# Performance work log

Measured on AMD Instinct MI355X. Metric: run time of the kernel, lower is better.

## Reference

```python
import jax, jax.numpy as jnp
import numpy as np

B, S, E, H = 8, 1024, 1024, 16
DK = E // H  # = n_wires = 64


def setup_inputs() -> dict:
    key = jax.random.key(0)
    k1, k2, k3 = jax.random.split(key, 3)
    x = jax.random.normal(k1, (B, S, E), dtype=jnp.float32)
    # trainable per-wire RX angles (shared across tokens and heads, as in QLayer)
    theta = jax.random.normal(k2, (DK,), dtype=jnp.float32)
    # combine_heads: nn.Linear(E, E, bias=False) -> weight [E, E], y = x @ W.T
    W_combine = (jax.random.normal(k3, (E, E), dtype=jnp.float32) / np.float32(np.sqrt(E)))
    return {"x": x, "theta": theta, "W_combine": W_combine}


def reference(x, theta, W_combine):
    # Quantum projection: per wire, RX(x_i) then RX(theta_i) on |0>, measure PauliZ.
    # RX(a)RX(b) = RX(a+b); <Z> of RX(a)|0> = cos(a)  =>  proj = cos(x + theta).
    b, s, e = x.shape
    xh = x.reshape(b, s, H, DK)            # [B, S, H, DK]
    proj = jnp.cos(xh + theta)             # product-state circuit, fully vectorized
    qkv = proj.transpose(0, 2, 1, 3)       # [B, H, S, DK]; q = k = v = proj

    scale = jnp.float32(1.0 / np.sqrt(DK))
    scores = jnp.einsum('bhqd,bhkd->bhqk', qkv, qkv) * scale  # [B, H, S, S]
    attn = jax.nn.softmax(scores, axis=-1)  # dropout disabled (eval / p=0)
    out = jnp.einsum('bhqk,bhkd->bhqd', attn, qkv)            # [B, H, S, DK]
    out = out.transpose(0, 2, 1, 3).reshape(b, s, e)          # [B, S, E]
    return out @ W_combine.T
```

## Files before the change

### kernel.cpp

```cpp
#include <hip/hip_runtime.h>
#include <hip/hip_bf16.h>
#include <stdint.h>

typedef float  f32x4   __attribute__((ext_vector_type(4)));
typedef float  f32x16  __attribute__((ext_vector_type(16)));
typedef __bf16 bf16x8  __attribute__((ext_vector_type(8)));
typedef __bf16 bf16x4  __attribute__((ext_vector_type(4)));

static constexpr int NB = 8, NS = 1024, NE = 1024, NH = 16;

#define MFMA16(a, b, c) __builtin_amdgcn_mfma_f32_16x16x32_bf16((a), (b), (c), 0, 0, 0)
#define MFMA32(a, b, c) __builtin_amdgcn_mfma_f32_32x32x16_bf16((a), (b), (c), 0, 0, 0)

__device__ __forceinline__ void gload_lds16(const void* g, void* l) {
    __builtin_amdgcn_global_load_lds(
        (const __attribute__((address_space(1))) void*)g,
        (__attribute__((address_space(3))) void*)l, 16, 0, 0);
}

__device__ __forceinline__ uint32_t cvt_pk_bf16(float lo, float hi) {
    uint32_t r;
    asm("v_cvt_pk_bf16_f32 %0, %1, %2" : "=v"(r) : "v"(lo), "v"(hi));
    return r;
}
__device__ __forceinline__ void pl32swap(uint32_t& a, uint32_t& b) {
    asm volatile("v_permlane32_swap_b32 %0, %1" : "+v"(a), "+v"(b));
}
__device__ __forceinline__ float exp2_raw(float x) {
    float r;
    asm("v_exp_f32 %0, %1" : "=v"(r) : "v"(x));
    return r;
}

__global__ __launch_bounds__(256) void k_proj(const float* __restrict__ x,
                                              const float* __restrict__ theta,
                                              __bf16* __restrict__ proj,
                                              __bf16* __restrict__ projT) {
    __shared__ float sm[64][65];
    const int bid  = blockIdx.x;
    const int bh   = bid >> 4;
    const int st0  = (bid & 15) << 6;
    const int b    = bh >> 4, h = bh & 15;
    const int t    = threadIdx.x;
    const int srow = t >> 2;
    const int j4   = t & 3;

    const float* xrow = x + ((size_t)(b * NS + st0 + srow)) * NE + h * 64;
    __bf16* prow = proj + ((size_t)bh * NS + st0 + srow) * 64;

#pragma unroll
    for (int k = 0; k < 4; ++k) {
        const int d = k * 16 + j4 * 4;
        float4 xv = *(const float4*)(xrow + d);
        float4 tv = *(const float4*)(theta + d);
        float c0 = __cosf(xv.x + tv.x);
        float c1 = __cosf(xv.y + tv.y);
        float c2 = __cosf(xv.z + tv.z);
        float c3 = __cosf(xv.w + tv.w);
        bf16x4 pv = {(__bf16)c0, (__bf16)c1, (__bf16)c2, (__bf16)c3};
        *(bf16x4*)(prow + d) = pv;
        sm[d + 0][srow] = c0;
        sm[d + 1][srow] = c1;
        sm[d + 2][srow] = c2;
        sm[d + 3][srow] = c3;
    }
    __syncthreads();

    const int drow = t >> 2;
    bf16x8 o0, o1;
#pragma unroll
    for (int i = 0; i < 8; ++i) {
        o0[i] = (__bf16)sm[drow][j4 * 16 + i];
        o1[i] = (__bf16)sm[drow][j4 * 16 + 8 + i];
    }
    __bf16* dst = projT + ((size_t)bh * 64 + drow) * NS + st0 + j4 * 16;
    *(bf16x8*)dst = o0;
    *(bf16x8*)(dst + 8) = o1;
}

__global__ __launch_bounds__(256) void k_cvtW(const float* __restrict__ W,
                                              __bf16* __restrict__ Wb) {
    const int i = (blockIdx.x * 256 + threadIdx.x) * 4;
    float4 v = *(const float4*)(W + i);
    bf16x4 o = {(__bf16)v.x, (__bf16)v.y, (__bf16)v.z, (__bf16)v.w};
    *(bf16x4*)(Wb + i) = o;
}

__global__ __launch_bounds__(256, 2) void k_attn(const __bf16* __restrict__ proj,
                                                 const __bf16* __restrict__ projT,
                                                 __bf16* __restrict__ attn_out) {
    __shared__ __align__(16) char smem[32768];
    __bf16* const smK0 = (__bf16*)(smem);
    __bf16* const smV0 = (__bf16*)(smem + 8192);
    __bf16* const smK1 = (__bf16*)(smem + 16384);
    __bf16* const smV1 = (__bf16*)(smem + 24576);

    const int bid  = blockIdx.x;
    const int bh   = bid >> 2;
    const int qblk = bid & 3;
    const int t    = threadIdx.x;
    const int w    = t >> 6;
    const int lane = t & 63;
    const int hi   = lane >> 5;
    const int l5   = lane & 31;
    const int l7   = l5 & 7;
    const int qw   = qblk * 256 + w * 64;

    const __bf16* P  = proj  + (size_t)bh * NS * 64;
    const __bf16* PT = projT + (size_t)bh * 64 * NS;

    const float csc = 0.18033688f;

    bf16x8 bq[2][4];
#pragma unroll
    for (int q01 = 0; q01 < 2; ++q01)
#pragma unroll
        for (int d = 0; d < 4; ++d) {
            bf16x8 v = *(const bf16x8*)(P + (size_t)(qw + q01 * 32 + l5) * 64 + d * 16 + hi * 8);
            bf16x8 o;
#pragma unroll
            for (int i = 0; i < 8; ++i) o[i] = (__bf16)((float)v[i] * csc);
            bq[q01][d] = o;
        }

    const __bf16* kP0[4];
    const __bf16* kP1[4];
    const __bf16* vP0[4];
    const __bf16* vP1[4];
#pragma unroll
    for (int d = 0; d < 4; ++d) {
        const int off = l5 * 64 + ((d * 2 + hi) ^ l7) * 8;
        kP0[d] = smK0 + off;
        kP1[d] = smK1 + off;
        vP0[d] = smV0 + off;
        vP1[d] = smV1 + off;
    }

    const int srow  = t >> 3;
    const int sjsrc = (t & 7) ^ (srow & 7);
    char* const dK0 = (char*)smK0 + t * 16;
    char* const dV0 = (char*)smV0 + t * 16;
    char* const dK1 = (char*)smK1 + t * 16;
    char* const dV1 = (char*)smV1 + t * 16;

#define STAGE(kvoff, dk, dv)                                                           \
    do {                                                                               \
        gload_lds16(P  + (size_t)((kvoff) + srow)      * 64 + sjsrc * 8, (dk));        \
        gload_lds16(P  + (size_t)((kvoff) + 32 + srow) * 64 + sjsrc * 8, (dk) + 4096); \
        gload_lds16(PT + (size_t)srow        * NS + (kvoff) + sjsrc * 8, (dv));        \
        gload_lds16(PT + (size_t)(32 + srow) * NS + (kvoff) + sjsrc * 8, (dv) + 4096); \
    } while (0)

    f32x16 acc0[2], acc1[2];
#pragma unroll
    for (int dt = 0; dt < 2; ++dt) {
        acc0[dt] = (f32x16){0.f,0.f,0.f,0.f,0.f,0.f,0.f,0.f,0.f,0.f,0.f,0.f,0.f,0.f,0.f,0.f};
        acc1[dt] = (f32x16){0.f,0.f,0.f,0.f,0.f,0.f,0.f,0.f,0.f,0.f,0.f,0.f,0.f,0.f,0.f,0.f};
    }
    float rs0 = 0.f, rs1 = 0.f;

    auto compute = [&](const __bf16* const* kR, const __bf16* const* vR) {
#pragma unroll
        for (int kt = 0; kt < 2; ++kt) {
            bf16x8 ak[4];
#pragma unroll
            for (int d = 0; d < 4; ++d)
                ak[d] = *(const bf16x8*)(kR[d] + kt * 2048);

            f32x16 st0 = (f32x16){0.f,0.f,0.f,0.f,0.f,0.f,0.f,0.f,0.f,0.f,0.f,0.f,0.f,0.f,0.f,0.f};
            f32x16 st1 = (f32x16){0.f,0.f,0.f,0.f,0.f,0.f,0.f,0.f,0.f,0.f,0.f,0.f,0.f,0.f,0.f,0.f};
            __builtin_amdgcn_s_setprio(1);
#pragma unroll
            for (int d = 0; d < 4; ++d) {
                st0 = MFMA32(ak[d], bq[0][d], st0);
                st1 = MFMA32(ak[d], bq[1][d], st1);
            }
            __builtin_amdgcn_s_setprio(0);

            uint32_t c0[8], c1[8];
            {
                float p[16];
#pragma unroll
                for (int r = 0; r < 16; ++r) p[r] = exp2_raw(st0[r]);
                rs0 += (((p[0] + p[1]) + (p[2] + p[3])) + ((p[4] + p[5]) + (p[6] + p[7]))) +
                       (((p[8] + p[9]) + (p[10] + p[11])) + ((p[12] + p[13]) + (p[14] + p[15])));
#pragma unroll
                for (int j = 0; j < 8; ++j) c0[j] = cvt_pk_bf16(p[2 * j], p[2 * j + 1]);
            }
            {
                float p[16];
#pragma unroll
                for (int r = 0; r < 16; ++r) p[r] = exp2_raw(st1[r]);
                rs1 += (((p[0] + p[1]) + (p[2] + p[3])) + ((p[4] + p[5]) + (p[6] + p[7]))) +
                       (((p[8] + p[9]) + (p[10] + p[11])) + ((p[12] + p[13]) + (p[14] + p[15])));
#pragma unroll
                for (int j = 0; j < 8; ++j) c1[j] = cvt_pk_bf16(p[2 * j], p[2 * j + 1]);
            }
            pl32swap(c0[0], c0[2]); pl32swap(c0[1], c0[3]);
            pl32swap(c0[4], c0[6]); pl32swap(c0[5], c0[7]);
            pl32swap(c1[0], c1[2]); pl32swap(c1[1], c1[3]);
            pl32swap(c1[4], c1[6]); pl32swap(c1[5], c1[7]);

#pragma unroll
            for (int half = 0; half < 2; ++half) {
                const int ks = kt * 2 + half;
                union U4 { uint32_t u[4]; bf16x8 v; };
                U4 f0, f1;
#pragma unroll
                for (int j = 0; j < 4; ++j) {
                    f0.u[j] = c0[half * 4 + j];
                    f1.u[j] = c1[half * 4 + j];
                }
                __builtin_amdgcn_s_setprio(1);
#pragma unroll
                for (int dt = 0; dt < 2; ++dt) {
                    bf16x8 av = *(const bf16x8*)(vR[ks] + dt * 2048);
                    acc0[dt] = MFMA32(av, f0.v, acc0[dt]);
                    acc1[dt] = MFMA32(av, f1.v, acc1[dt]);
                }
                __builtin_amdgcn_s_setprio(0);
            }
        }
    };

    STAGE(0, dK0, dV0);
    __syncthreads();

#pragma unroll 1
    for (int it2 = 0; it2 < 8; ++it2) {
        STAGE((2 * it2 + 1) * 64, dK1, dV1);
        compute(kP0, vP0);
        __syncthreads();
        if (it2 < 7) STAGE((2 * it2 + 2) * 64, dK0, dV0);
        compute(kP1, vP1);
        __syncthreads();
    }
#undef STAGE

    float* const epw = (float*)smem + w * (32 * 33);
    const int orow = lane >> 1;
    const int ohalf = lane & 1;

#pragma unroll
    for (int q01 = 0; q01 < 2; ++q01) {
        float rs = (q01 == 0) ? rs0 : rs1;
        rs += __shfl_xor(rs, 32);
        const float inv = 1.0f / rs;
#pragma unroll
        for (int dt = 0; dt < 2; ++dt) {
            const f32x16 a = (q01 == 0) ? acc0[dt] : acc1[dt];
#pragma unroll
            for (int r = 0; r < 16; ++r)
                epw[l5 * 33 + (r & 3) + 8 * (r >> 2) + 4 * hi] = a[r] * inv;
            bf16x8 o0, o1;
#pragma unroll
            for (int i = 0; i < 8; ++i) {
                o0[i] = (__bf16)(epw[orow * 33 + ohalf * 16 + i]);
                o1[i] = (__bf16)(epw[orow * 33 + ohalf * 16 + 8 + i]);
            }
            __bf16* dst = attn_out +
                ((size_t)(bh >> 4) * NS + qblk * 256 + w * 64 + q01 * 32 + orow) * NE +
                (bh & 15) * 64 + dt * 32 + ohalf * 16;
            *(bf16x8*)dst = o0;
            *(bf16x8*)(dst + 8) = o1;
        }
    }
}

__global__ __launch_bounds__(256) void k_gemm(const __bf16* __restrict__ A,
                                              const __bf16* __restrict__ Bw,
                                              float* __restrict__ C) {
    constexpr int K = 1024, N = 1024;
    __shared__ __bf16 As[128 * 32];
    __shared__ __bf16 Bs[128 * 32];

    const int t = threadIdx.x;
    const int lane = t & 63, w = t >> 6;
    const int g = lane >> 4, c = lane & 15;
    const int wr = w >> 1, wc = w & 1;
    const size_t row0 = (size_t)blockIdx.x * 128;
    const size_t col0 = (size_t)blockIdx.y * 128;

    const char* Ag = (const char*)(A + row0 * K);
    const char* Bg = (const char*)(Bw + col0 * K);
    char* AsB = (char*)As;
    char* BsB = (char*)Bs;
    const int srow  = t >> 2;
    const int sbyte = (t & 3) * 16;

    f32x4 acc[4][4];
#pragma unroll
    for (int m = 0; m < 4; ++m)
#pragma unroll
        for (int n = 0; n < 4; ++n) acc[m][n] = (f32x4){0.f, 0.f, 0.f, 0.f};

    for (int kb = 0; kb < K; kb += 32) {
        gload_lds16(Ag + (size_t)srow * (K * 2) + kb * 2 + sbyte, AsB + t * 16);
        gload_lds16(Ag + (size_t)(srow + 64) * (K * 2) + kb * 2 + sbyte, AsB + 4096 + t * 16);
        gload_lds16(Bg + (size_t)srow * (K * 2) + kb * 2 + sbyte, BsB + t * 16);
        gload_lds16(Bg + (size_t)(srow + 64) * (K * 2) + kb * 2 + sbyte, BsB + 4096 + t * 16);
        __syncthreads();

        bf16x8 a[4], b[4];
#pragma unroll
        for (int m = 0; m < 4; ++m)
            a[m] = *(const bf16x8*)(As + (wr * 64 + m * 16 + c) * 32 + g * 8);
#pragma unroll
        for (int n = 0; n < 4; ++n)
            b[n] = *(const bf16x8*)(Bs + (wc * 64 + n * 16 + c) * 32 + g * 8);
#pragma unroll
        for (int m = 0; m < 4; ++m)
#pragma unroll
            for (int n = 0; n < 4; ++n) acc[m][n] = MFMA16(a[m], b[n], acc[m][n]);
        __syncthreads();
    }

#pragma unroll
    for (int m = 0; m < 4; ++m)
#pragma unroll
        for (int n = 0; n < 4; ++n)
#pragma unroll
            for (int r = 0; r < 4; ++r)
                C[(row0 + wr * 64 + m * 16 + 4 * g + r) * N + col0 + wc * 64 + n * 16 + c] =
                    acc[m][n][r];
}

extern "C" void kernel_launch(void* const* d_in, const int* in_sizes, int n_in,
                              void* d_out, int out_size, void* d_ws, size_t ws_size,
                              hipStream_t stream) {
    const float* x     = (const float*)d_in[0];
    const float* theta = (const float*)d_in[1];
    const float* W     = (const float*)d_in[2];
    float* out = (float*)d_out;

    char* ws = (char*)d_ws;
    __bf16* proj  = (__bf16*)(ws);
    __bf16* projT = (__bf16*)(ws + 16777216);
    __bf16* Wb    = (__bf16*)(ws + 33554432);
    __bf16* ao    = (__bf16*)(ws + 35651584);

    k_proj<<<NB * NH * (NS / 64), 256, 0, stream>>>(x, theta, proj, projT);
    k_cvtW<<<(NE * NE / 4) / 256, 256, 0, stream>>>(W, Wb);
    k_attn<<<NB * NH * 4, 256, 0, stream>>>(proj, projT, ao);
    dim3 gg(NB * NS / 128, NE / 128);
    k_gemm<<<gg, 256, 0, stream>>>(ao, Wb, out);
}
```

Baseline: 84.06 us.

## Halve per-warp query rows, double attention grid, recompute Q from x

Each warp in the attention kernel now handles 32 query rows instead of 64, so the grid grows from 512 to 1024 blocks and launch bounds allow 4 blocks per SM, aiming for higher occupancy and better load balance. The block index is remapped so that consecutive blocks take different heads and query blocks are in the outer position. Q fragments are recomputed directly from x and theta with __cosf rather than read from the bf16 proj buffer. In exchange, K/V tiles are loaded into LDS twice as often per query, and the fast cosine plus bf16 rounding of Q may change numerics slightly.

```diff
diff --git a/kernel.cpp b/kernel.cpp
--- a/kernel.cpp
+++ b/kernel.cpp
@@ -86,7 +86,9 @@
     *(bf16x4*)(Wb + i) = o;
 }
 
-__global__ __launch_bounds__(256, 2) void k_attn(const __bf16* __restrict__ proj,
+__global__ __launch_bounds__(256, 4) void k_attn(const float* __restrict__ x,
+                                                 const float* __restrict__ theta,
+                                                 const __bf16* __restrict__ proj,
                                                  const __bf16* __restrict__ projT,
                                                  __bf16* __restrict__ attn_out) {
     __shared__ __align__(16) char smem[32768];
@@ -96,32 +98,44 @@
     __bf16* const smV1 = (__bf16*)(smem + 24576);
 
     const int bid  = blockIdx.x;
-    const int bh   = bid >> 2;
-    const int qblk = bid & 3;
+    const int bh   = (bid & 7) + 8 * ((bid >> 3) & 15);
+    const int qblk = bid >> 7;
     const int t    = threadIdx.x;
     const int w    = t >> 6;
     const int lane = t & 63;
     const int hi   = lane >> 5;
     const int l5   = lane & 31;
     const int l7   = l5 & 7;
-    const int qw   = qblk * 256 + w * 64;
+    const int qw   = qblk * 128 + w * 32;
+    const int b    = bh >> 4, h = bh & 15;
 
     const __bf16* P  = proj  + (size_t)bh * NS * 64;
     const __bf16* PT = projT + (size_t)bh * 64 * NS;
 
     const float csc = 0.18033688f;
 
-    bf16x8 bq[2][4];
-#pragma unroll
-    for (int q01 = 0; q01 < 2; ++q01)
+    bf16x8 bq[4];
+    {
+        const float* xr = x + ((size_t)(b * NS + qw + l5)) * NE + h * 64;
 #pragma unroll
         for (int d = 0; d < 4; ++d) {
-            bf16x8 v = *(const bf16x8*)(P + (size_t)(qw + q01 * 32 + l5) * 64 + d * 16 + hi * 8);
+            const int d0 = d * 16 + hi * 8;
+            float4 x0 = *(const float4*)(xr + d0);
+            float4 x1 = *(const float4*)(xr + d0 + 4);
+            float4 t0 = *(const float4*)(theta + d0);
+            float4 t1 = *(const float4*)(theta + d0 + 4);
             bf16x8 o;
-#pragma unroll
-            for (int i = 0; i < 8; ++i) o[i] = (__bf16)((float)v[i] * csc);
-            bq[q01][d] = o;
+            o[0] = (__bf16)(__cosf(x0.x + t0.x) * csc);
+            o[1] = (__bf16)(__cosf(x0.y + t0.y) * csc);
+            o[2] = (__bf16)(__cosf(x0.z + t0.z) * csc);
+            o[3] = (__bf16)(__cosf(x0.w + t0.w) * csc);
+            o[4] = (__bf16)(__cosf(x1.x + t1.x) * csc);
+            o[5] = (__bf16)(__cosf(x1.y + t1.y) * csc);
+            o[6] = (__bf16)(__cosf(x1.z + t1.z) * csc);
+            o[7] = (__bf16)(__cosf(x1.w + t1.w) * csc);
+            bq[d] = o;
         }
+    }
 
     const __bf16* kP0[4];
     const __bf16* kP1[4];
@@ -151,13 +165,11 @@
         gload_lds16(PT + (size_t)(32 + srow) * NS + (kvoff) + sjsrc * 8, (dv) + 4096); \
     } while (0)
 
-    f32x16 acc0[2], acc1[2];
-#pragma unroll
-    for (int dt = 0; dt < 2; ++dt) {
-        acc0[dt] = (f32x16){0.f,0.f,0.f,0.f,0.f,0.f,0.f,0.f,0.f,0.f,0.f,0.f,0.f,0.f,0.f,0.f};
-        acc1[dt] = (f32x16){0.f,0.f,0.f,0.f,0.f,0.f,0.f,0.f,0.f,0.f,0.f,0.f,0.f,0.f,0.f,0.f};
-    }
-    float rs0 = 0.f, rs1 = 0.f;
+    f32x16 acc[2];
+#pragma unroll
+    for (int dt = 0; dt < 2; ++dt)
+        acc[dt] = (f32x16){0.f,0.f,0.f,0.f,0.f,0.f,0.f,0.f,0.f,0.f,0.f,0.f,0.f,0.f,0.f,0.f};
+    float rs = 0.f;
 
     auto compute = [&](const __bf16* const* kR, const __bf16* const* vR) {
 #pragma unroll
@@ -167,56 +179,34 @@
             for (int d = 0; d < 4; ++d)
                 ak[d] = *(const bf16x8*)(kR[d] + kt * 2048);
 
-            f32x16 st0 = (f32x16){0.f,0.f,0.f,0.f,0.f,0.f,0.f,0.f,0.f,0.f,0.f,0.f,0.f,0.f,0.f,0.f};
-            f32x16 st1 = (f32x16){0.f,0.f,0.f,0.f,0.f,0.f,0.f,0.f,0.f,0.f,0.f,0.f,0.f,0.f,0.f,0.f};
+            f32x16 st = (f32x16){0.f,0.f,0.f,0.f,0.f,0.f,0.f,0.f,0.f,0.f,0.f,0.f,0.f,0.f,0.f,0.f};
             __builtin_amdgcn_s_setprio(1);
 #pragma unroll
-            for (int d = 0; d < 4; ++d) {
-                st0 = MFMA32(ak[d], bq[0][d], st0);
-                st1 = MFMA32(ak[d], bq[1][d], st1);
-            }
+            for (int d = 0; d < 4; ++d) st = MFMA32(ak[d], bq[d], st);
             __builtin_amdgcn_s_setprio(0);
 
-            uint32_t c0[8], c1[8];
-            {
-                float p[16];
-#pragma unroll
-                for (int r = 0; r < 16; ++r) p[r] = exp2_raw(st0[r]);
-                rs0 += (((p[0] + p[1]) + (p[2] + p[3])) + ((p[4] + p[5]) + (p[6] + p[7]))) +
-                       (((p[8] + p[9]) + (p[10] + p[11])) + ((p[12] + p[13]) + (p[14] + p[15])));
-#pragma unroll
-                for (int j = 0; j < 8; ++j) c0[j] = cvt_pk_bf16(p[2 * j], p[2 * j + 1]);
-            }
-            {
-                float p[16];
-#pragma unroll
-                for (int r = 0; r < 16; ++r) p[r] = exp2_raw(st1[r]);
-                rs1 += (((p[0] + p[1]) + (p[2] + p[3])) + ((p[4] + p[5]) + (p[6] + p[7]))) +
-                       (((p[8] + p[9]) + (p[10] + p[11])) + ((p[12] + p[13]) + (p[14] + p[15])));
-#pragma unroll
-                for (int j = 0; j < 8; ++j) c1[j] = cvt_pk_bf16(p[2 * j], p[2 * j + 1]);
-            }
+            float p[16];
+#pragma unroll
+            for (int r = 0; r < 16; ++r) p[r] = exp2_raw(st[r]);
+            rs += (((p[0] + p[1]) + (p[2] + p[3])) + ((p[4] + p[5]) + (p[6] + p[7]))) +
+                  (((p[8] + p[9]) + (p[10] + p[11])) + ((p[12] + p[13]) + (p[14] + p[15])));
+            uint32_t c0[8];
+#pragma unroll
+            for (int j = 0; j < 8; ++j) c0[j] = cvt_pk_bf16(p[2 * j], p[2 * j + 1]);
             pl32swap(c0[0], c0[2]); pl32swap(c0[1], c0[3]);
             pl32swap(c0[4], c0[6]); pl32swap(c0[5], c0[7]);
-            pl32swap(c1[0], c1[2]); pl32swap(c1[1], c1[3]);
-            pl32swap(c1[4], c1[6]); pl32swap(c1[5], c1[7]);
 
 #pragma unroll
             for (int half = 0; half < 2; ++half) {
                 const int ks = kt * 2 + half;
-                union U4 { uint32_t u[4]; bf16x8 v; };
-                U4 f0, f1;
-#pragma unroll
-                for (int j = 0; j < 4; ++j) {
-                    f0.u[j] = c0[half * 4 + j];
-                    f1.u[j] = c1[half * 4 + j];
-                }
+                union U4 { uint32_t u[4]; bf16x8 v; } f0;
+#pragma unroll
+                for (int j = 0; j < 4; ++j) f0.u[j] = c0[half * 4 + j];
                 __builtin_amdgcn_s_setprio(1);
 #pragma unroll
                 for (int dt = 0; dt < 2; ++dt) {
                     bf16x8 av = *(const bf16x8*)(vR[ks] + dt * 2048);
-                    acc0[dt] = MFMA32(av, f0.v, acc0[dt]);
-                    acc1[dt] = MFMA32(av, f1.v, acc1[dt]);
+                    acc[dt] = MFMA32(av, f0.v, acc[dt]);
                 }
                 __builtin_amdgcn_s_setprio(0);
             }
@@ -241,29 +231,25 @@
     const int orow = lane >> 1;
     const int ohalf = lane & 1;
 
-#pragma unroll
-    for (int q01 = 0; q01 < 2; ++q01) {
-        float rs = (q01 == 0) ? rs0 : rs1;
-        rs += __shfl_xor(rs, 32);
-        const float inv = 1.0f / rs;
-#pragma unroll
-        for (int dt = 0; dt < 2; ++dt) {
-            const f32x16 a = (q01 == 0) ? acc0[dt] : acc1[dt];
-#pragma unroll
-            for (int r = 0; r < 16; ++r)
-                epw[l5 * 33 + (r & 3) + 8 * (r >> 2) + 4 * hi] = a[r] * inv;
-            bf16x8 o0, o1;
-#pragma unroll
-            for (int i = 0; i < 8; ++i) {
-                o0[i] = (__bf16)(epw[orow * 33 + ohalf * 16 + i]);
-                o1[i] = (__bf16)(epw[orow * 33 + ohalf * 16 + 8 + i]);
-            }
-            __bf16* dst = attn_out +
-                ((size_t)(bh >> 4) * NS + qblk * 256 + w * 64 + q01 * 32 + orow) * NE +
-                (bh & 15) * 64 + dt * 32 + ohalf * 16;
-            *(bf16x8*)dst = o0;
-            *(bf16x8*)(dst + 8) = o1;
+    rs += __shfl_xor(rs, 32);
+    const float inv = 1.0f / rs;
+#pragma unroll
+    for (int dt = 0; dt < 2; ++dt) {
+        const f32x16 a = acc[dt];
+#pragma unroll
+        for (int r = 0; r < 16; ++r)
+            epw[l5 * 33 + (r & 3) + 8 * (r >> 2) + 4 * hi] = a[r] * inv;
+        bf16x8 o0, o1;
+#pragma unroll
+        for (int i = 0; i < 8; ++i) {
+            o0[i] = (__bf16)(epw[orow * 33 + ohalf * 16 + i]);
+            o1[i] = (__bf16)(epw[orow * 33 + ohalf * 16 + 8 + i]);
         }
+        __bf16* dst = attn_out +
+            ((size_t)b * NS + qblk * 128 + w * 32 + orow) * NE +
+            h * 64 + dt * 32 + ohalf * 16;
+        *(bf16x8*)dst = o0;
+        *(bf16x8*)(dst + 8) = o1;
     }
 }
 
@@ -341,7 +327,7 @@
 
     k_proj<<<NB * NH * (NS / 64), 256, 0, stream>>>(x, theta, proj, projT);
     k_cvtW<<<(NE * NE / 4) / 256, 256, 0, stream>>>(W, Wb);
-    k_attn<<<NB * NH * 4, 256, 0, stream>>>(proj, projT, ao);
+    k_attn<<<NB * NH * 8, 256, 0, stream>>>(x, theta, proj, projT, ao);
     dim3 gg(NB * NS / 128, NE / 128);
     k_gemm<<<gg, 256, 0, stream>>>(ao, Wb, out);
 }
```

Result: slower. 87.82 us (+4.5%).

## Triple-buffer K/V tiles with vmcnt waits and remap block-to-head order

Applied to the files above, without the earlier changes.

Replaces the double-buffered K/V staging, which used two __syncthreads per pair of tiles, with a three-buffer rotation. Each phase waits on vmcnt for the oldest load group, issues one barrier, then prefetches two tiles ahead, so loads and compute overlap more deeply. Blocks are remapped so consecutive block IDs cover different heads at the same query block. The score scale moves from pre-scaling Q in bf16 to multiplying scores before exp2. The cost is 48KB of LDS per block, which may limit the occupancy of two blocks per CU, plus extra multiplies in the softmax loop.

```diff
diff --git a/kernel.cpp b/kernel.cpp
--- a/kernel.cpp
+++ b/kernel.cpp
@@ -89,15 +89,17 @@
 __global__ __launch_bounds__(256, 2) void k_attn(const __bf16* __restrict__ proj,
                                                  const __bf16* __restrict__ projT,
                                                  __bf16* __restrict__ attn_out) {
-    __shared__ __align__(16) char smem[32768];
+    __shared__ __align__(16) char smem[49152];
     __bf16* const smK0 = (__bf16*)(smem);
     __bf16* const smV0 = (__bf16*)(smem + 8192);
     __bf16* const smK1 = (__bf16*)(smem + 16384);
     __bf16* const smV1 = (__bf16*)(smem + 24576);
+    __bf16* const smK2 = (__bf16*)(smem + 32768);
+    __bf16* const smV2 = (__bf16*)(smem + 40960);
 
     const int bid  = blockIdx.x;
-    const int bh   = bid >> 2;
-    const int qblk = bid & 3;
+    const int bh   = (bid & 7) + 8 * ((bid >> 3) & 15);
+    const int qblk = bid >> 7;
     const int t    = threadIdx.x;
     const int w    = t >> 6;
     const int lane = t & 63;
@@ -105,6 +107,7 @@
     const int l5   = lane & 31;
     const int l7   = l5 & 7;
     const int qw   = qblk * 256 + w * 64;
+    const int b    = bh >> 4, h = bh & 15;
 
     const __bf16* P  = proj  + (size_t)bh * NS * 64;
     const __bf16* PT = projT + (size_t)bh * 64 * NS;
@@ -115,33 +118,21 @@
 #pragma unroll
     for (int q01 = 0; q01 < 2; ++q01)
 #pragma unroll
-        for (int d = 0; d < 4; ++d) {
-            bf16x8 v = *(const bf16x8*)(P + (size_t)(qw + q01 * 32 + l5) * 64 + d * 16 + hi * 8);
-            bf16x8 o;
-#pragma unroll
-            for (int i = 0; i < 8; ++i) o[i] = (__bf16)((float)v[i] * csc);
-            bq[q01][d] = o;
-        }
-
-    const __bf16* kP0[4];
-    const __bf16* kP1[4];
-    const __bf16* vP0[4];
-    const __bf16* vP1[4];
-#pragma unroll
-    for (int d = 0; d < 4; ++d) {
-        const int off = l5 * 64 + ((d * 2 + hi) ^ l7) * 8;
-        kP0[d] = smK0 + off;
-        kP1[d] = smK1 + off;
-        vP0[d] = smV0 + off;
-        vP1[d] = smV1 + off;
-    }
+        for (int d = 0; d < 4; ++d)
+            bq[q01][d] = *(const bf16x8*)(P + (size_t)(qw + q01 * 32 + l5) * 64 + d * 16 + hi * 8);
+
+    int roff[4];
+#pragma unroll
+    for (int d = 0; d < 4; ++d) roff[d] = l5 * 64 + ((d * 2 + hi) ^ l7) * 8;
 
     const int srow  = t >> 3;
     const int sjsrc = (t & 7) ^ (srow & 7);
-    char* const dK0 = (char*)smK0 + t * 16;
-    char* const dV0 = (char*)smV0 + t * 16;
-    char* const dK1 = (char*)smK1 + t * 16;
-    char* const dV1 = (char*)smV1 + t * 16;
+    char* const sdK0 = (char*)smK0 + t * 16;
+    char* const sdV0 = (char*)smV0 + t * 16;
+    char* const sdK1 = (char*)smK1 + t * 16;
+    char* const sdV1 = (char*)smV1 + t * 16;
+    char* const sdK2 = (char*)smK2 + t * 16;
+    char* const sdV2 = (char*)smV2 + t * 16;
 
 #define STAGE(kvoff, dk, dv)                                                           \
     do {                                                                               \
@@ -159,13 +150,13 @@
     }
     float rs0 = 0.f, rs1 = 0.f;
 
-    auto compute = [&](const __bf16* const* kR, const __bf16* const* vR) {
+    auto computeTile = [&](const __bf16* kB, const __bf16* vB) {
 #pragma unroll
         for (int kt = 0; kt < 2; ++kt) {
             bf16x8 ak[4];
 #pragma unroll
             for (int d = 0; d < 4; ++d)
-                ak[d] = *(const bf16x8*)(kR[d] + kt * 2048);
+                ak[d] = *(const bf16x8*)(kB + roff[d] + kt * 2048);
 
             f32x16 st0 = (f32x16){0.f,0.f,0.f,0.f,0.f,0.f,0.f,0.f,0.f,0.f,0.f,0.f,0.f,0.f,0.f,0.f};
             f32x16 st1 = (f32x16){0.f,0.f,0.f,0.f,0.f,0.f,0.f,0.f,0.f,0.f,0.f,0.f,0.f,0.f,0.f,0.f};
@@ -181,7 +172,7 @@
             {
                 float p[16];
 #pragma unroll
-                for (int r = 0; r < 16; ++r) p[r] = exp2_raw(st0[r]);
+                for (int r = 0; r < 16; ++r) p[r] = exp2_raw(st0[r] * csc);
                 rs0 += (((p[0] + p[1]) + (p[2] + p[3])) + ((p[4] + p[5]) + (p[6] + p[7]))) +
                        (((p[8] + p[9]) + (p[10] + p[11])) + ((p[12] + p[13]) + (p[14] + p[15])));
 #pragma unroll
@@ -190,7 +181,7 @@
             {
                 float p[16];
 #pragma unroll
-                for (int r = 0; r < 16; ++r) p[r] = exp2_raw(st1[r]);
+                for (int r = 0; r < 16; ++r) p[r] = exp2_raw(st1[r] * csc);
                 rs1 += (((p[0] + p[1]) + (p[2] + p[3])) + ((p[4] + p[5]) + (p[6] + p[7]))) +
                        (((p[8] + p[9]) + (p[10] + p[11])) + ((p[12] + p[13]) + (p[14] + p[15])));
 #pragma unroll
@@ -214,7 +205,7 @@
                 __builtin_amdgcn_s_setprio(1);
 #pragma unroll
                 for (int dt = 0; dt < 2; ++dt) {
-                    bf16x8 av = *(const bf16x8*)(vR[ks] + dt * 2048);
+                    bf16x8 av = *(const bf16x8*)(vB + roff[ks] + dt * 2048);
                     acc0[dt] = MFMA32(av, f0.v, acc0[dt]);
                     acc1[dt] = MFMA32(av, f1.v, acc1[dt]);
                 }
@@ -223,19 +214,33 @@
         }
     };
 
-    STAGE(0, dK0, dV0);
-    __syncthreads();
+#define PHASE(IT, CUR, NXT, WAITN)                                        \
+    do {                                                                  \
+        asm volatile("s_waitcnt vmcnt(" #WAITN ")" ::: "memory");         \
+        __builtin_amdgcn_sched_barrier(0);                                \
+        __builtin_amdgcn_s_barrier();                                     \
+        __builtin_amdgcn_sched_barrier(0);                                \
+        if ((IT) < 14) STAGE(((IT) + 2) * 64, sdK##NXT, sdV##NXT);        \
+        computeTile(smK##CUR, smV##CUR);                                  \
+    } while (0)
+
+    STAGE(0, sdK0, sdV0);
+    STAGE(64, sdK1, sdV1);
 
 #pragma unroll 1
-    for (int it2 = 0; it2 < 8; ++it2) {
-        STAGE((2 * it2 + 1) * 64, dK1, dV1);
-        compute(kP0, vP0);
-        __syncthreads();
-        if (it2 < 7) STAGE((2 * it2 + 2) * 64, dK0, dV0);
-        compute(kP1, vP1);
-        __syncthreads();
-    }
+    for (int g3 = 0; g3 < 5; ++g3) {
+        const int it0 = g3 * 3;
+        PHASE(it0 + 0, 0, 2, 4);
+        PHASE(it0 + 1, 1, 0, 4);
+        PHASE(it0 + 2, 2, 1, 4);
+    }
+    PHASE(15, 0, 2, 0);
+
+#undef PHASE
 #undef STAGE
+
+    __builtin_amdgcn_sched_barrier(0);
+    __builtin_amdgcn_s_barrier();
 
     float* const epw = (float*)smem + w * (32 * 33);
     const int orow = lane >> 1;
@@ -259,8 +264,8 @@
                 o1[i] = (__bf16)(epw[orow * 33 + ohalf * 16 + 8 + i]);
             }
             __bf16* dst = attn_out +
-                ((size_t)(bh >> 4) * NS + qblk * 256 + w * 64 + q01 * 32 + orow) * NE +
-                (bh & 15) * 64 + dt * 32 + ohalf * 16;
+                ((size_t)b * NS + qblk * 256 + w * 64 + q01 * 32 + orow) * NE +
+                h * 64 + dt * 32 + ohalf * 16;
             *(bf16x8*)dst = o0;
             *(bf16x8*)(dst + 8) = o1;
         }
```

After: 99.39 us. 18.2% more time.
